# Performance work log

Measured on AMD Instinct MI355X. Metric: run time of the kernel, lower is better.

## Reference

```python
import jax, jax.numpy as jnp
import numpy as np
from jax import lax

# Problem constants (match input_specs): 16 clouds x 4096 points, ratio 0.25
N = 65536
B = 16
N_PER = 4096
RATIO = 0.25
M = int(N_PER * RATIO)  # 1024 sampled points per cloud
D = 512                 # feature dim


def setup_inputs() -> dict:
    key = jax.random.key(0)
    kx, kp = jax.random.split(key)
    x = jax.random.normal(kx, (N, D), dtype=jnp.float32)
    pos = jax.random.normal(kp, (N, 3), dtype=jnp.float32)
    # contiguous equal-sized batches, as produced by a PyG DataLoader with equal cloud sizes
    batch = (jnp.arange(N) // N_PER).astype(jnp.int32)
    return {"x": x, "pos": pos, "batch": batch}


def _fps_one(pos_b):
    """Farthest point sampling on one cloud. pos_b: [N_PER, 3] -> local idx [M] int32.
    Deterministic start at point 0 (torch_cluster.fps with random_start=False)."""
    big = jnp.asarray(1e30, pos_b.dtype)

    def step(carry, _):
        dist, last = carry
        d2 = jnp.sum((pos_b - pos_b[last]) ** 2, axis=-1)  # [N_PER]
        dist = jnp.minimum(dist, d2)
        nxt = jnp.argmax(dist).astype(jnp.int32)
        return (dist, nxt), nxt

    init = (jnp.full((pos_b.shape[0],), big, pos_b.dtype), jnp.int32(0))
    _, rest = lax.scan(step, init, None, length=M - 1)  # [M-1]
    return jnp.concatenate([jnp.zeros((1,), jnp.int32), rest])


def reference(x, pos, batch):
    # per-cloud FPS (batches are contiguous and equal-sized)
    pos_b = pos.reshape(B, N_PER, 3)
    local = jax.vmap(_fps_one)(pos_b)  # [B, M]
    offs = (jnp.arange(B, dtype=jnp.int32) * N_PER)[:, None]
    idx = (local + offs).reshape(-1)   # [B*M] global indices
    # irregular gather of x / pos / batch, as in GraphPool.forward
    return x[idx], pos[idx], batch[idx]
```

## Files before the change

### kernel.cpp

```cpp
#include <hip/hip_runtime.h>

#define N_PER   4096
#define M_SAMP  1024
#define B_CL    16
#define D_FEAT  512
#define TPB     256
#define NWAVE   (TPB / 64)
#define PPT     (N_PER / TPB)
#define NPAIR   (PPT / 2)

typedef float v2f __attribute__((ext_vector_type(2)));

template <int CTRL>
__device__ __forceinline__ void dpp_combine2(unsigned& khi, unsigned& klo) {
    unsigned h2 = (unsigned)__builtin_amdgcn_update_dpp((int)khi, (int)khi, CTRL, 0xF, 0xF, false);
    unsigned l2 = (unsigned)__builtin_amdgcn_update_dpp((int)klo, (int)klo, CTRL, 0xF, 0xF, false);
    unsigned long long k  = ((unsigned long long)khi << 32) | klo;
    unsigned long long k2 = ((unsigned long long)h2  << 32) | l2;
    if (k2 > k) { khi = h2; klo = l2; }
}

__global__ __launch_bounds__(TPB)
__attribute__((amdgpu_waves_per_eu(1, 1)))
void fps_kernel(const float* __restrict__ pos, int* __restrict__ sidx) {
    __shared__ float4             spos[N_PER];
    __shared__ unsigned long long sw[2][NWAVE];
    __shared__ int                sloc[M_SAMP];

    const int cloud = blockIdx.x;
    const int tid   = threadIdx.x;
    const float* posb = pos + (size_t)cloud * N_PER * 3;

    v2f px2[NPAIR], py2[NPAIR], pz2[NPAIR], dist2[NPAIR];
    const int base = tid * PPT;
    {
        float f[48];
        const float4* posb4 = (const float4*)posb + tid * 12;
#pragma unroll
        for (int v = 0; v < 12; ++v) {
            float4 t = posb4[v];
            f[4 * v + 0] = t.x; f[4 * v + 1] = t.y;
            f[4 * v + 2] = t.z; f[4 * v + 3] = t.w;
        }
#pragma unroll
        for (int p = 0; p < NPAIR; ++p) {
            px2[p] = (v2f){f[6 * p + 0], f[6 * p + 3]};
            py2[p] = (v2f){f[6 * p + 1], f[6 * p + 4]};
            pz2[p] = (v2f){f[6 * p + 2], f[6 * p + 5]};
            dist2[p] = (v2f){1e30f, 1e30f};
        }
#pragma unroll
        for (int j = 0; j < PPT; ++j)
            spos[base + j] = make_float4(f[3 * j], f[3 * j + 1], f[3 * j + 2], 0.0f);
    }

    float lx = posb[0], ly = posb[1], lz = posb[2];
    if (tid == 0) sloc[0] = 0;

    const int wave = tid >> 6;
    const int lane = tid & 63;
    __syncthreads();

    for (int s = 1; s < M_SAMP; ++s) {
        float bv = -1.0f;
        int   bj = 0;
        v2f lxv = {lx, lx}, lyv = {ly, ly}, lzv = {lz, lz};
#pragma unroll
        for (int p = 0; p < NPAIR; ++p) {
#pragma clang fp contract(off)
            v2f dx = px2[p] - lxv;
            v2f dy = py2[p] - lyv;
            v2f dz = pz2[p] - lzv;
            v2f d2 = dx * dx + dy * dy + dz * dz;
            v2f dn = __builtin_elementwise_min(dist2[p], d2);
            dist2[p] = dn;
            bool t0 = dn.x > bv; bv = t0 ? dn.x : bv; bj = t0 ? 2 * p     : bj;
            bool t1 = dn.y > bv; bv = t1 ? dn.y : bv; bj = t1 ? 2 * p + 1 : bj;
        }
        unsigned khi = __float_as_uint(bv);
        unsigned klo = (unsigned)(N_PER - 1 - (base + bj));

        dpp_combine2<0xB1>(khi, klo);
        dpp_combine2<0x4E>(khi, klo);
        dpp_combine2<0x141>(khi, klo);
        dpp_combine2<0x140>(khi, klo);
        dpp_combine2<0x142>(khi, klo);
        dpp_combine2<0x143>(khi, klo);

        const int buf = s & 1;
        if (lane == 63) sw[buf][wave] = ((unsigned long long)khi << 32) | klo;
        __syncthreads();

        unsigned long long k = sw[buf][0];
#pragma unroll
        for (int w = 1; w < NWAVE; ++w) {
            unsigned long long k2 = sw[buf][w];
            if (k2 > k) k = k2;
        }
        int widx = N_PER - 1 - (int)(unsigned)(k & 0xFFFFFFFFu);
        float4 wp = spos[widx];
        lx = wp.x; ly = wp.y; lz = wp.z;
        if (tid == 0) sloc[s] = widx;
    }

    __syncthreads();
    for (int i = tid; i < M_SAMP; i += TPB)
        sidx[cloud * M_SAMP + i] = sloc[i];
}

__global__ __launch_bounds__(256) void gather_x_kernel(const float4* __restrict__ x4,
                                                       const int* __restrict__ sidx,
                                                       float4* __restrict__ out4) {
    int id = blockIdx.x * 256 + threadIdx.x;
    int r  = id >> 7;
    int c  = id & 127;
    int g  = sidx[r] + (r >> 10 << 12);
    out4[id] = x4[(size_t)g * (D_FEAT / 4) + c];
}

__global__ __launch_bounds__(256) void gather_pb_kernel(const float* __restrict__ pos,
                                                        const int* __restrict__ batch,
                                                        const int* __restrict__ sidx,
                                                        float* __restrict__ out_pos,
                                                        float* __restrict__ out_batch) {
    int r = blockIdx.x * 256 + threadIdx.x;
    int g = sidx[r] + (r >> 10 << 12);
    out_pos[r * 3 + 0] = pos[g * 3 + 0];
    out_pos[r * 3 + 1] = pos[g * 3 + 1];
    out_pos[r * 3 + 2] = pos[g * 3 + 2];
    out_batch[r] = (float)batch[g];
}

extern "C" void kernel_launch(void* const* d_in, const int* in_sizes, int n_in,
                              void* d_out, int out_size, void* d_ws, size_t ws_size,
                              hipStream_t stream) {
    const float* x     = (const float*)d_in[0];
    const float* pos   = (const float*)d_in[1];
    const int*   batch = (const int*)d_in[2];

    int* sidx = (int*)d_ws;

    float* out   = (float*)d_out;
    float* out_x = out;
    float* out_p = out + (size_t)B_CL * M_SAMP * D_FEAT;
    float* out_b = out_p + (size_t)B_CL * M_SAMP * 3;

    fps_kernel<<<B_CL, TPB, 0, stream>>>(pos, sidx);

    gather_x_kernel<<<(B_CL * M_SAMP * (D_FEAT / 4)) / 256, 256, 0, stream>>>(
        (const float4*)x, sidx, (float4*)out_x);

    gather_pb_kernel<<<(B_CL * M_SAMP) / 256, 256, 0, stream>>>(
        pos, batch, sidx, out_p, out_b);
}
```

Before: 750.1 us.

## Process two clouds per FPS block and carry winner coordinates through reduction

Each FPS block now handles two clouds with interleaved independent steps, so one barrier per iteration covers both clouds. The aim is to hide the latency of the serial argmax chain and the barrier. The DPP and cross-wave reductions now carry the winning point's coordinates, which removes the shared-memory position table and its lookup. The two gather kernels are merged into one launch. In exchange, register pressure doubles and only 8 blocks run on the GPU.

```diff
diff --git a/kernel.cpp b/kernel.cpp
--- a/kernel.cpp
+++ b/kernel.cpp
@@ -8,127 +8,190 @@
 #define NWAVE   (TPB / 64)
 #define PPT     (N_PER / TPB)
 #define NPAIR   (PPT / 2)
+#define CPW     2
 
 typedef float v2f __attribute__((ext_vector_type(2)));
 
 template <int CTRL>
-__device__ __forceinline__ void dpp_combine2(unsigned& khi, unsigned& klo) {
+__device__ __forceinline__ void dpp_combine5(unsigned& khi, unsigned& klo,
+                                             float& x, float& y, float& z) {
     unsigned h2 = (unsigned)__builtin_amdgcn_update_dpp((int)khi, (int)khi, CTRL, 0xF, 0xF, false);
     unsigned l2 = (unsigned)__builtin_amdgcn_update_dpp((int)klo, (int)klo, CTRL, 0xF, 0xF, false);
+    int xi = __builtin_amdgcn_update_dpp(__float_as_int(x), __float_as_int(x), CTRL, 0xF, 0xF, false);
+    int yi = __builtin_amdgcn_update_dpp(__float_as_int(y), __float_as_int(y), CTRL, 0xF, 0xF, false);
+    int zi = __builtin_amdgcn_update_dpp(__float_as_int(z), __float_as_int(z), CTRL, 0xF, 0xF, false);
     unsigned long long k  = ((unsigned long long)khi << 32) | klo;
     unsigned long long k2 = ((unsigned long long)h2  << 32) | l2;
-    if (k2 > k) { khi = h2; klo = l2; }
+    if (k2 > k) {
+        khi = h2; klo = l2;
+        x = __int_as_float(xi); y = __int_as_float(yi); z = __int_as_float(zi);
+    }
+}
+
+__device__ __forceinline__ void fps_step(const v2f (&px2)[NPAIR], const v2f (&py2)[NPAIR],
+                                         const v2f (&pz2)[NPAIR], v2f (&dist2)[NPAIR],
+                                         float lx, float ly, float lz, int base,
+                                         unsigned& khi, unsigned& klo,
+                                         float& cx, float& cy, float& cz) {
+    float bv = -1.0f;
+    int   bj = 0;
+    float bx = px2[0].x, by = py2[0].x, bz = pz2[0].x;
+    v2f lxv = {lx, lx}, lyv = {ly, ly}, lzv = {lz, lz};
+#pragma unroll
+    for (int p = 0; p < NPAIR; ++p) {
+#pragma clang fp contract(off)
+        v2f dx = px2[p] - lxv;
+        v2f dy = py2[p] - lyv;
+        v2f dz = pz2[p] - lzv;
+        v2f d2 = dx * dx + dy * dy + dz * dz;
+        v2f dn = __builtin_elementwise_min(dist2[p], d2);
+        dist2[p] = dn;
+        bool t0 = dn.x > bv;
+        bv = t0 ? dn.x : bv; bj = t0 ? 2 * p : bj;
+        bx = t0 ? px2[p].x : bx; by = t0 ? py2[p].x : by; bz = t0 ? pz2[p].x : bz;
+        bool t1 = dn.y > bv;
+        bv = t1 ? dn.y : bv; bj = t1 ? 2 * p + 1 : bj;
+        bx = t1 ? px2[p].y : bx; by = t1 ? py2[p].y : by; bz = t1 ? pz2[p].y : bz;
+    }
+    khi = __float_as_uint(bv);
+    klo = (unsigned)(N_PER - 1 - (base + bj));
+    cx = bx; cy = by; cz = bz;
+    dpp_combine5<0xB1>(khi, klo, cx, cy, cz);
+    dpp_combine5<0x4E>(khi, klo, cx, cy, cz);
+    dpp_combine5<0x141>(khi, klo, cx, cy, cz);
+    dpp_combine5<0x140>(khi, klo, cx, cy, cz);
+    dpp_combine5<0x142>(khi, klo, cx, cy, cz);
+    dpp_combine5<0x143>(khi, klo, cx, cy, cz);
 }
 
 __global__ __launch_bounds__(TPB)
 __attribute__((amdgpu_waves_per_eu(1, 1)))
 void fps_kernel(const float* __restrict__ pos, int* __restrict__ sidx) {
-    __shared__ float4             spos[N_PER];
-    __shared__ unsigned long long sw[2][NWAVE];
-    __shared__ int                sloc[M_SAMP];
-
-    const int cloud = blockIdx.x;
-    const int tid   = threadIdx.x;
-    const float* posb = pos + (size_t)cloud * N_PER * 3;
-
-    v2f px2[NPAIR], py2[NPAIR], pz2[NPAIR], dist2[NPAIR];
+    __shared__ uint4 sw4[CPW][2][NWAVE];
+    __shared__ float swz[CPW][2][NWAVE];
+    __shared__ int   sloc[CPW][M_SAMP];
+
+    const int tid    = threadIdx.x;
+    const int cloudA = blockIdx.x * CPW;
+    const int cloudB = cloudA + 1;
+    const float* posA = pos + (size_t)cloudA * N_PER * 3;
+    const float* posB = pos + (size_t)cloudB * N_PER * 3;
     const int base = tid * PPT;
+
+    v2f pxA[NPAIR], pyA[NPAIR], pzA[NPAIR], dA[NPAIR];
+    v2f pxB[NPAIR], pyB[NPAIR], pzB[NPAIR], dB[NPAIR];
     {
         float f[48];
-        const float4* posb4 = (const float4*)posb + tid * 12;
+        const float4* p4 = (const float4*)posA + tid * 12;
 #pragma unroll
         for (int v = 0; v < 12; ++v) {
-            float4 t = posb4[v];
-            f[4 * v + 0] = t.x; f[4 * v + 1] = t.y;
-            f[4 * v + 2] = t.z; f[4 * v + 3] = t.w;
+            float4 t = p4[v];
+            f[4 * v] = t.x; f[4 * v + 1] = t.y; f[4 * v + 2] = t.z; f[4 * v + 3] = t.w;
         }
 #pragma unroll
         for (int p = 0; p < NPAIR; ++p) {
-            px2[p] = (v2f){f[6 * p + 0], f[6 * p + 3]};
-            py2[p] = (v2f){f[6 * p + 1], f[6 * p + 4]};
-            pz2[p] = (v2f){f[6 * p + 2], f[6 * p + 5]};
-            dist2[p] = (v2f){1e30f, 1e30f};
-        }
-#pragma unroll
-        for (int j = 0; j < PPT; ++j)
-            spos[base + j] = make_float4(f[3 * j], f[3 * j + 1], f[3 * j + 2], 0.0f);
-    }
-
-    float lx = posb[0], ly = posb[1], lz = posb[2];
-    if (tid == 0) sloc[0] = 0;
+            pxA[p] = (v2f){f[6 * p], f[6 * p + 3]};
+            pyA[p] = (v2f){f[6 * p + 1], f[6 * p + 4]};
+            pzA[p] = (v2f){f[6 * p + 2], f[6 * p + 5]};
+            dA[p] = (v2f){1e30f, 1e30f};
+        }
+        p4 = (const float4*)posB + tid * 12;
+#pragma unroll
+        for (int v = 0; v < 12; ++v) {
+            float4 t = p4[v];
+            f[4 * v] = t.x; f[4 * v + 1] = t.y; f[4 * v + 2] = t.z; f[4 * v + 3] = t.w;
+        }
+#pragma unroll
+        for (int p = 0; p < NPAIR; ++p) {
+            pxB[p] = (v2f){f[6 * p], f[6 * p + 3]};
+            pyB[p] = (v2f){f[6 * p + 1], f[6 * p + 4]};
+            pzB[p] = (v2f){f[6 * p + 2], f[6 * p + 5]};
+            dB[p] = (v2f){1e30f, 1e30f};
+        }
+    }
+
+    float lxA = posA[0], lyA = posA[1], lzA = posA[2];
+    float lxB = posB[0], lyB = posB[1], lzB = posB[2];
+    if (tid == 0) { sloc[0][0] = 0; sloc[1][0] = 0; }
 
     const int wave = tid >> 6;
     const int lane = tid & 63;
+
+    for (int s = 1; s < M_SAMP; ++s) {
+        const int buf = s & 1;
+        {
+            unsigned khi, klo; float cx, cy, cz;
+            fps_step(pxA, pyA, pzA, dA, lxA, lyA, lzA, base, khi, klo, cx, cy, cz);
+            if (lane == 63) {
+                sw4[0][buf][wave] = make_uint4(khi, klo, __float_as_uint(cx), __float_as_uint(cy));
+                swz[0][buf][wave] = cz;
+            }
+        }
+        {
+            unsigned khi, klo; float cx, cy, cz;
+            fps_step(pxB, pyB, pzB, dB, lxB, lyB, lzB, base, khi, klo, cx, cy, cz);
+            if (lane == 63) {
+                sw4[1][buf][wave] = make_uint4(khi, klo, __float_as_uint(cx), __float_as_uint(cy));
+                swz[1][buf][wave] = cz;
+            }
+        }
+        __syncthreads();
+
+        {
+            uint4 m = sw4[0][buf][0]; float mz = swz[0][buf][0];
+#pragma unroll
+            for (int w = 1; w < NWAVE; ++w) {
+                uint4 t = sw4[0][buf][w]; float tz = swz[0][buf][w];
+                unsigned long long k  = ((unsigned long long)m.x << 32) | m.y;
+                unsigned long long k2 = ((unsigned long long)t.x << 32) | t.y;
+                if (k2 > k) { m = t; mz = tz; }
+            }
+            lxA = __uint_as_float(m.z); lyA = __uint_as_float(m.w); lzA = mz;
+            if (tid == 0) sloc[0][s] = N_PER - 1 - (int)m.y;
+        }
+        {
+            uint4 m = sw4[1][buf][0]; float mz = swz[1][buf][0];
+#pragma unroll
+            for (int w = 1; w < NWAVE; ++w) {
+                uint4 t = sw4[1][buf][w]; float tz = swz[1][buf][w];
+                unsigned long long k  = ((unsigned long long)m.x << 32) | m.y;
+                unsigned long long k2 = ((unsigned long long)t.x << 32) | t.y;
+                if (k2 > k) { m = t; mz = tz; }
+            }
+            lxB = __uint_as_float(m.z); lyB = __uint_as_float(m.w); lzB = mz;
+            if (tid == 0) sloc[1][s] = N_PER - 1 - (int)m.y;
+        }
+    }
+
     __syncthreads();
-
-    for (int s = 1; s < M_SAMP; ++s) {
-        float bv = -1.0f;
-        int   bj = 0;
-        v2f lxv = {lx, lx}, lyv = {ly, ly}, lzv = {lz, lz};
-#pragma unroll
-        for (int p = 0; p < NPAIR; ++p) {
-#pragma clang fp contract(off)
-            v2f dx = px2[p] - lxv;
-            v2f dy = py2[p] - lyv;
-            v2f dz = pz2[p] - lzv;
-            v2f d2 = dx * dx + dy * dy + dz * dz;
-            v2f dn = __builtin_elementwise_min(dist2[p], d2);
-            dist2[p] = dn;
-            bool t0 = dn.x > bv; bv = t0 ? dn.x : bv; bj = t0 ? 2 * p     : bj;
-            bool t1 = dn.y > bv; bv = t1 ? dn.y : bv; bj = t1 ? 2 * p + 1 : bj;
-        }
-        unsigned khi = __float_as_uint(bv);
-        unsigned klo = (unsigned)(N_PER - 1 - (base + bj));
-
-        dpp_combine2<0xB1>(khi, klo);
-        dpp_combine2<0x4E>(khi, klo);
-        dpp_combine2<0x141>(khi, klo);
-        dpp_combine2<0x140>(khi, klo);
-        dpp_combine2<0x142>(khi, klo);
-        dpp_combine2<0x143>(khi, klo);
-
-        const int buf = s & 1;
-        if (lane == 63) sw[buf][wave] = ((unsigned long long)khi << 32) | klo;
-        __syncthreads();
-
-        unsigned long long k = sw[buf][0];
-#pragma unroll
-        for (int w = 1; w < NWAVE; ++w) {
-            unsigned long long k2 = sw[buf][w];
-            if (k2 > k) k = k2;
-        }
-        int widx = N_PER - 1 - (int)(unsigned)(k & 0xFFFFFFFFu);
-        float4 wp = spos[widx];
-        lx = wp.x; ly = wp.y; lz = wp.z;
-        if (tid == 0) sloc[s] = widx;
-    }
-
-    __syncthreads();
-    for (int i = tid; i < M_SAMP; i += TPB)
-        sidx[cloud * M_SAMP + i] = sloc[i];
-}
-
-__global__ __launch_bounds__(256) void gather_x_kernel(const float4* __restrict__ x4,
-                                                       const int* __restrict__ sidx,
-                                                       float4* __restrict__ out4) {
-    int id = blockIdx.x * 256 + threadIdx.x;
-    int r  = id >> 7;
-    int c  = id & 127;
-    int g  = sidx[r] + (r >> 10 << 12);
-    out4[id] = x4[(size_t)g * (D_FEAT / 4) + c];
-}
-
-__global__ __launch_bounds__(256) void gather_pb_kernel(const float* __restrict__ pos,
-                                                        const int* __restrict__ batch,
-                                                        const int* __restrict__ sidx,
-                                                        float* __restrict__ out_pos,
-                                                        float* __restrict__ out_batch) {
-    int r = blockIdx.x * 256 + threadIdx.x;
-    int g = sidx[r] + (r >> 10 << 12);
-    out_pos[r * 3 + 0] = pos[g * 3 + 0];
-    out_pos[r * 3 + 1] = pos[g * 3 + 1];
-    out_pos[r * 3 + 2] = pos[g * 3 + 2];
-    out_batch[r] = (float)batch[g];
+    for (int i = tid; i < M_SAMP; i += TPB) {
+        sidx[cloudA * M_SAMP + i] = sloc[0][i];
+        sidx[cloudB * M_SAMP + i] = sloc[1][i];
+    }
+}
+
+__global__ __launch_bounds__(256) void gather_kernel(const float4* __restrict__ x4,
+                                                     const float* __restrict__ pos,
+                                                     const int* __restrict__ batch,
+                                                     const int* __restrict__ sidx,
+                                                     float4* __restrict__ out4,
+                                                     float* __restrict__ out_pos,
+                                                     float* __restrict__ out_batch) {
+    int b = blockIdx.x;
+    if (b < 8192) {
+        int id = b * 256 + threadIdx.x;
+        int r  = id >> 7;
+        int c  = id & 127;
+        int g  = sidx[r] + (r >> 10 << 12);
+        out4[id] = x4[(size_t)g * (D_FEAT / 4) + c];
+    } else {
+        int r = (b - 8192) * 256 + threadIdx.x;
+        int g = sidx[r] + (r >> 10 << 12);
+        out_pos[r * 3 + 0] = pos[g * 3 + 0];
+        out_pos[r * 3 + 1] = pos[g * 3 + 1];
+        out_pos[r * 3 + 2] = pos[g * 3 + 2];
+        out_batch[r] = (float)batch[g];
+    }
 }
 
 extern "C" void kernel_launch(void* const* d_in, const int* in_sizes, int n_in,
@@ -145,11 +208,8 @@
     float* out_p = out + (size_t)B_CL * M_SAMP * D_FEAT;
     float* out_b = out_p + (size_t)B_CL * M_SAMP * 3;
 
-    fps_kernel<<<B_CL, TPB, 0, stream>>>(pos, sidx);
-
-    gather_x_kernel<<<(B_CL * M_SAMP * (D_FEAT / 4)) / 256, 256, 0, stream>>>(
-        (const float4*)x, sidx, (float4*)out_x);
-
-    gather_pb_kernel<<<(B_CL * M_SAMP) / 256, 256, 0, stream>>>(
-        pos, batch, sidx, out_p, out_b);
-}
+    fps_kernel<<<B_CL / CPW, TPB, 0, stream>>>(pos, sidx);
+
+    gather_kernel<<<8192 + 64, 256, 0, stream>>>(
+        (const float4*)x, pos, batch, sidx, (float4*)out_x, out_p, out_b);
+}
```

New measurement: 2.056 ms. +174.2%, slower.
